# Kernel optimization log

Measured on AMD Instinct MI355X. Metric: run time of the kernel, lower is better.

The kernel has to match this reference:

```python
import jax, jax.numpy as jnp
import numpy as np

TEMPERATURE = 0.5


def _neg_indices(b):
    # Static (numpy) reconstruction of _get_correlated_mask for using_teacher=False:
    # mask excludes the diagonal and the +b/-b (mod 2b) positive-pair entries.
    n = 2 * b
    eye = np.eye(n, dtype=np.uint8)
    mask = (1 - (eye + np.roll(eye, -b, axis=1))).astype(bool)
    cols = np.broadcast_to(np.arange(n), (n, n))
    # torch's sim[mask].view(2b, -1) flattens row-major, so per-row sorted column order.
    return jnp.asarray(cols[mask].reshape(n, n - 2))  # [2b, 2b-2] int32


def setup_inputs() -> dict:
    key = jax.random.key(0)
    k1, k2 = jax.random.split(key)
    zis = jax.random.normal(k1, (4096, 256), dtype=jnp.float32)
    zjs = jax.random.normal(k2, (4096, 256), dtype=jnp.float32)
    return {"zis": zis, "zjs": zjs}


def reference(zis, zjs):
    b = zis.shape[0]
    reps = jnp.concatenate([zjs, zis], axis=0)              # [2b, d]
    sim = reps @ reps.T                                      # [2b, 2b] dot-product similarity
    # positives: sim[i, i+b] for i<b, then sim[i+b, i] -> sim[i, (i+b) mod 2b]
    l_pos = jnp.diagonal(sim, offset=b)
    r_pos = jnp.diagonal(sim, offset=-b)
    positives = jnp.concatenate([l_pos, r_pos])[:, None]     # [2b, 1]
    neg_idx = _neg_indices(b)
    negatives = jnp.take_along_axis(sim, neg_idx, axis=1)    # [2b, 2b-2]
    logits = jnp.concatenate([positives, negatives], axis=1) / TEMPERATURE
    # CrossEntropyLoss(reduction='sum') with labels all zero
    loss = jnp.sum(jax.nn.logsumexp(logits, axis=1) - logits[:, 0])
    accuracy = jnp.mean((jnp.argmax(logits, axis=1) == 0).astype(jnp.float32))
    return (loss / (2 * b), accuracy)
```

## Files before the change

kernel.cpp:

```cpp
#include <hip/hip_runtime.h>
#include <hip/hip_bf16.h>

#define N_TOT  8192
#define B_HALF 4096
#define D_DIM  256
#define NSPLIT 32
#define MFIX   192.0f

typedef short bf16x8 __attribute__((ext_vector_type(8)));
typedef float f32x4  __attribute__((ext_vector_type(4)));

#define NEG_INF (-__builtin_inff())
#define RSCALE  1.6986436f
#define LN2F    0.69314718056f

__device__ __forceinline__ float exp2_fast(float x) {
  float r;
  asm("v_exp_f32 %0, %1" : "=v"(r) : "v"(x));
  return r;
}

__device__ __forceinline__ unsigned short f2b(float f) {
  __hip_bfloat16 h = __float2bfloat16(f);
  return *reinterpret_cast<unsigned short*>(&h);
}

__global__ __launch_bounds__(256) void convert_k(const float* __restrict__ zis,
                                                 const float* __restrict__ zjs,
                                                 unsigned short* __restrict__ reps,
                                                 float* __restrict__ out) {
  size_t idx = ((size_t)blockIdx.x * 256 + threadIdx.x) * 4;
  const float* src = (idx < (size_t)B_HALF * D_DIM) ? (zjs + idx)
                                                    : (zis + (idx - (size_t)B_HALF * D_DIM));
  float4 v = *reinterpret_cast<const float4*>(src);
  ushort4 o;
  o.x = f2b(v.x * RSCALE); o.y = f2b(v.y * RSCALE);
  o.z = f2b(v.z * RSCALE); o.w = f2b(v.w * RSCALE);
  *reinterpret_cast<ushort4*>(reps + idx) = o;
  if (blockIdx.x == 0 && threadIdx.x < 2) out[threadIdx.x] = 0.0f;
}

#define G2L(srcp, ldsp)                                                          \
  __builtin_amdgcn_global_load_lds(                                              \
      (const __attribute__((address_space(1))) void*)(srcp),                     \
      (__attribute__((address_space(3))) void*)(ldsp), 16, 0, 0)

__global__ __launch_bounds__(512, 2) void ntxent_main(const unsigned short* __restrict__ reps,
                                                      float* __restrict__ part_m,
                                                      float* __restrict__ part_s,
                                                      float* __restrict__ pos_out) {
  __shared__ short As[2][16384];
  __shared__ short Bs[2][16384];

  const int tid  = threadIdx.x;
  const int lane = tid & 63;
  const int l15  = lane & 15;
  const int l4   = lane >> 4;
  const int wave = tid >> 6;
  const int wr   = wave >> 2;
  const int wc   = wave & 3;

  const unsigned wg = (blockIdx.x & 7) * 128 + (blockIdx.x >> 3);
  const int bx = wg >> 5, by = wg & 31;
  const int R0 = bx * 256, C0 = by * 256;
  const bool dblk = (bx == by);
  const bool pblk = (by == ((bx + 16) & 31));

#define ISSUE_A(h, slot, kt)                                                        \
  do {                                                                              \
    _Pragma("unroll") for (int j_ = 0; j_ < 2; ++j_) {                              \
      const int u_ = tid >> 3;                                                      \
      const unsigned short* s_ = reps + (size_t)(R0 + j_ * 128 + (h) * 64 + u_) * D_DIM \
                                 + (kt) * 64 + (((tid & 7) ^ (u_ & 7)) * 8);        \
      G2L(s_, &As[slot][(((h) * 2 + j_) * 512 + tid) * 8]);                         \
    }                                                                               \
  } while (0)

#define ISSUE_B(g, slot, kt)                                                        \
  do {                                                                              \
    _Pragma("unroll") for (int j_ = 0; j_ < 2; ++j_) {                              \
      const int u_ = tid >> 3;                                                      \
      const int col_ = (u_ & 31) + (g) * 32 + (((j_ * 2) + (u_ >> 5)) & 3) * 64;    \
      const unsigned short* s_ = reps + (size_t)(C0 + col_) * D_DIM                 \
                                 + (kt) * 64 + (((tid & 7) ^ (u_ & 7)) * 8);        \
      G2L(s_, &Bs[slot][(((g) * 2 + j_) * 512 + tid) * 8]);                         \
    }                                                                               \
  } while (0)

#define READ_A(h, slot)                                                             \
  do {                                                                              \
    _Pragma("unroll") for (int mf = 0; mf < 4; ++mf)                                \
      _Pragma("unroll") for (int kk = 0; kk < 2; ++kk)                              \
        af[mf][kk] = *reinterpret_cast<const bf16x8*>(                              \
            &As[slot][((h) * 128 + wr * 64 + mf * 16 + l15) * 64 +                  \
                      (((kk * 4 + l4) ^ (l15 & 7)) * 8)]);                          \
  } while (0)

#define READ_B(g, dst, slot)                                                        \
  do {                                                                              \
    _Pragma("unroll") for (int nf = 0; nf < 2; ++nf)                                \
      _Pragma("unroll") for (int kk = 0; kk < 2; ++kk)                              \
        dst[nf][kk] = *reinterpret_cast<const bf16x8*>(                             \
            &Bs[slot][((g) * 128 + wc * 32 + nf * 16 + l15) * 64 +                  \
                      (((kk * 4 + l4) ^ (l15 & 7)) * 8)]);                          \
  } while (0)

#define MFMA_Q(h, g, bfx)                                                           \
  do {                                                                              \
    _Pragma("unroll") for (int mf = 0; mf < 4; ++mf)                                \
      _Pragma("unroll") for (int nf = 0; nf < 2; ++nf)                              \
        _Pragma("unroll") for (int kk = 0; kk < 2; ++kk)                            \
          acc[h][g][mf][nf] = __builtin_amdgcn_mfma_f32_16x16x32_bf16(              \
              af[mf][kk], bfx[nf][kk], acc[h][g][mf][nf], 0, 0, 0);                 \
  } while (0)

#define PHASE_MID()                                          \
  do {                                                       \
    __builtin_amdgcn_s_barrier();                            \
    asm volatile("s_waitcnt lgkmcnt(0)" ::: "memory");       \
    __builtin_amdgcn_sched_barrier(0);                       \
    __builtin_amdgcn_s_setprio(1);                           \
  } while (0)

#define PHASE_END_G(n)                                       \
  do {                                                       \
    __builtin_amdgcn_s_setprio(0);                           \
    asm volatile("s_waitcnt vmcnt(" #n ")" ::: "memory");    \
    __builtin_amdgcn_s_barrier();                            \
  } while (0)

#define PHASE_END_NOG()                                      \
  do {                                                       \
    __builtin_amdgcn_s_setprio(0);                           \
    __builtin_amdgcn_s_barrier();                            \
  } while (0)

  f32x4 acc[2][2][4][2];
  const f32x4 vz = {0.f, 0.f, 0.f, 0.f};
#pragma unroll
  for (int h = 0; h < 2; ++h)
#pragma unroll
    for (int g = 0; g < 2; ++g)
#pragma unroll
      for (int mf = 0; mf < 4; ++mf)
#pragma unroll
        for (int nf = 0; nf < 2; ++nf) acc[h][g][mf][nf] = vz;

  bf16x8 af[4][2], bf0[2][2], bf1[2][2];

  ISSUE_A(0, 0, 0); ISSUE_B(0, 0, 0); ISSUE_B(1, 0, 0); ISSUE_A(1, 0, 0);
  asm volatile("s_waitcnt vmcnt(4)" ::: "memory");
  __builtin_amdgcn_s_barrier();

#pragma unroll
  for (int t = 0; t < 3; ++t) {
    const int sl = t & 1, sn = sl ^ 1, kn = t + 1;
    READ_A(0, sl); READ_B(0, bf0, sl); ISSUE_A(0, sn, kn);
    PHASE_MID(); MFMA_Q(0, 0, bf0); PHASE_END_G(4);
    READ_B(1, bf1, sl); ISSUE_B(0, sn, kn);
    PHASE_MID(); MFMA_Q(0, 1, bf1); PHASE_END_G(4);
    READ_A(1, sl); ISSUE_B(1, sn, kn);
    PHASE_MID(); MFMA_Q(1, 1, bf1); PHASE_END_NOG();
    ISSUE_A(1, sn, kn);
    PHASE_MID(); MFMA_Q(1, 0, bf0); PHASE_END_G(4);
  }
  READ_A(0, 1); READ_B(0, bf0, 1);
  PHASE_MID(); MFMA_Q(0, 0, bf0); PHASE_END_G(2);
  READ_B(1, bf1, 1);
  PHASE_MID(); MFMA_Q(0, 1, bf1); PHASE_END_G(0);
  READ_A(1, 1);
  PHASE_MID(); MFMA_Q(1, 1, bf1); PHASE_END_NOG();
  PHASE_MID(); MFMA_Q(1, 0, bf0);
  __builtin_amdgcn_s_setprio(0);

  __syncthreads();
  float2* red = reinterpret_cast<float2*>(&Bs[0][0]);
  float posv[2][4];
#pragma unroll
  for (int h = 0; h < 2; ++h)
#pragma unroll
    for (int mf = 0; mf < 4; ++mf) posv[h][mf] = NEG_INF;

#pragma unroll
  for (int h = 0; h < 2; ++h) {
#pragma unroll
    for (int mf = 0; mf < 4; ++mf) {
#pragma unroll
      for (int r = 0; r < 4; ++r) {
        float m_ = NEG_INF, s_ = 0.f;
#pragma unroll
        for (int g = 0; g < 2; ++g) {
#pragma unroll
          for (int nf = 0; nf < 2; ++nf) {
            float v = acc[h][g][mf][nf][r];
            const bool hit16 = (8 * wr + 4 * h + mf) == (4 * wc + 2 * g + nf);
            if (hit16 && l15 == l4 * 4 + r) {
              if (dblk) v = NEG_INF;
              if (pblk) posv[h][mf] = v;
            }
            m_ = fmaxf(m_, v);
            s_ += exp2_fast(v - MFIX);
          }
        }
#pragma unroll
        for (int off = 1; off < 16; off <<= 1) {
          s_ += __shfl_xor(s_, off, 16);
          m_ = fmaxf(m_, __shfl_xor(m_, off, 16));
        }
        if (l15 == 0)
          red[(wr * 128 + h * 64 + mf * 16 + l4 * 4 + r) * 4 + wc] = make_float2(m_, s_);
      }
    }
  }
  __syncthreads();
  if (tid < 256) {
    float2 p0 = red[tid * 4 + 0], p1 = red[tid * 4 + 1];
    float2 p2 = red[tid * 4 + 2], p3 = red[tid * 4 + 3];
    const int i = R0 + tid;
    part_m[i * NSPLIT + by] = fmaxf(fmaxf(p0.x, p1.x), fmaxf(p2.x, p3.x));
    part_s[i * NSPLIT + by] = p0.y + p1.y + p2.y + p3.y;
  }
  if (pblk) {
#pragma unroll
    for (int h = 0; h < 2; ++h) {
#pragma unroll
      for (int mf = 0; mf < 4; ++mf) {
        const bool valid = (unsigned)(8 * wr + 4 * h + mf - 4 * wc) < 4u;
#pragma unroll
        for (int r = 0; r < 4; ++r) {
          float p = __shfl(posv[h][mf], (lane & 48) + l4 * 4 + r, 64);
          if (valid && l15 == 0)
            pos_out[R0 + wr * 128 + h * 64 + mf * 16 + l4 * 4 + r] = p;
        }
      }
    }
  }
}

__global__ __launch_bounds__(256) void finalize_k(const float* __restrict__ pm,
                                                  const float* __restrict__ ps,
                                                  const float* __restrict__ pv,
                                                  float* __restrict__ out) {
  const int row = blockIdx.x * 256 + threadIdx.x;
  float m = NEG_INF, ss = 0.f;
#pragma unroll
  for (int s = 0; s < NSPLIT; ++s) {
    m  = fmaxf(m, pm[row * NSPLIT + s]);
    ss += ps[row * NSPLIT + s];
  }
  const float posu = pv[row];
  float loss = (MFIX + __log2f(ss) - posu) * LN2F;
  float hit  = (posu >= m) ? 1.0f : 0.0f;

#pragma unroll
  for (int off = 32; off; off >>= 1) {
    loss += __shfl_down(loss, off);
    hit  += __shfl_down(hit,  off);
  }
  __shared__ float redL[4], redH[4];
  const int wv = threadIdx.x >> 6;
  if ((threadIdx.x & 63) == 0) { redL[wv] = loss; redH[wv] = hit; }
  __syncthreads();
  if (threadIdx.x == 0) {
    float L = redL[0] + redL[1] + redL[2] + redL[3];
    float H = redH[0] + redH[1] + redH[2] + redH[3];
    atomicAdd(&out[0], L * (1.0f / 8192.0f));
    atomicAdd(&out[1], H * (1.0f / 8192.0f));
  }
}

extern "C" void kernel_launch(void* const* d_in, const int* in_sizes, int n_in,
                              void* d_out, int out_size, void* d_ws, size_t ws_size,
                              hipStream_t stream) {
  const float* zis = (const float*)d_in[0];
  const float* zjs = (const float*)d_in[1];
  float* out = (float*)d_out;

  char* ws = (char*)d_ws;
  unsigned short* reps = (unsigned short*)ws;
  float* part_m = (float*)(ws + 4u * 1024u * 1024u);
  float* part_s = (float*)(ws + 5u * 1024u * 1024u);
  float* pos_a  = (float*)(ws + 6u * 1024u * 1024u);
  (void)in_sizes; (void)n_in; (void)out_size; (void)ws_size;

  convert_k<<<2048, 256, 0, stream>>>(zis, zjs, reps, out);
  ntxent_main<<<1024, 512, 0, stream>>>(reps, part_m, part_s, pos_a);
  finalize_k<<<32, 256, 0, stream>>>(part_m, part_s, pos_a, out);
}
```

Measured before the change: 129.0 us.

## Make GEMM workgroups persistent over four column tiles and fuse finalize via last-block reduction

New measurement: 208.0 us. 1.61x slower.

```diff
diff --git a/kernel.cpp b/kernel.cpp
--- a/kernel.cpp
+++ b/kernel.cpp
@@ -4,7 +4,7 @@
 #define N_TOT  8192
 #define B_HALF 4096
 #define D_DIM  256
-#define NSPLIT 32
+#define PARTW  8
 #define MFIX   192.0f
 
 typedef short bf16x8 __attribute__((ext_vector_type(8)));
@@ -28,7 +28,8 @@
 __global__ __launch_bounds__(256) void convert_k(const float* __restrict__ zis,
                                                  const float* __restrict__ zjs,
                                                  unsigned short* __restrict__ reps,
-                                                 float* __restrict__ out) {
+                                                 float* __restrict__ out,
+                                                 int* __restrict__ counter) {
   size_t idx = ((size_t)blockIdx.x * 256 + threadIdx.x) * 4;
   const float* src = (idx < (size_t)B_HALF * D_DIM) ? (zjs + idx)
                                                     : (zis + (idx - (size_t)B_HALF * D_DIM));
@@ -38,6 +39,7 @@
   o.z = f2b(v.z * RSCALE); o.w = f2b(v.w * RSCALE);
   *reinterpret_cast<ushort4*>(reps + idx) = o;
   if (blockIdx.x == 0 && threadIdx.x < 2) out[threadIdx.x] = 0.0f;
+  if (blockIdx.x == 0 && threadIdx.x == 2) *counter = 0;
 }
 
 #define G2L(srcp, ldsp)                                                          \
@@ -48,9 +50,11 @@
 __global__ __launch_bounds__(512, 2) void ntxent_main(const unsigned short* __restrict__ reps,
                                                       float* __restrict__ part_m,
                                                       float* __restrict__ part_s,
-                                                      float* __restrict__ pos_out) {
-  __shared__ short As[2][16384];
-  __shared__ short Bs[2][16384];
+                                                      float* __restrict__ pos_out,
+                                                      int* __restrict__ counter,
+                                                      float* __restrict__ out) {
+  __shared__ short As[32768];
+  __shared__ short Bs[32768];
 
   const int tid  = threadIdx.x;
   const int lane = tid & 63;
@@ -60,49 +64,53 @@
   const int wr   = wave >> 2;
   const int wc   = wave & 3;
 
-  const unsigned wg = (blockIdx.x & 7) * 128 + (blockIdx.x >> 3);
-  const int bx = wg >> 5, by = wg & 31;
-  const int R0 = bx * 256, C0 = by * 256;
-  const bool dblk = (bx == by);
-  const bool pblk = (by == ((bx + 16) & 31));
-
-#define ISSUE_A(h, slot, kt)                                                        \
+  const int xcd  = (int)blockIdx.x & 7;
+  const int idx  = (int)blockIdx.x >> 3;
+  const int rp   = (xcd & 3) * 8 + (idx >> 2);
+  const int cg   = (xcd >> 2) * 4 + (idx & 3);
+  const int R0   = rp * 256;
+  const int G0   = cg * 1024;
+  const bool dblk = (cg == (rp >> 2));
+  const bool pblk = (cg == (((rp >> 2) + 4) & 7));
+  const int  sct  = rp & 3;
+
+#define ISSUE_A(hh, sbase, ko)                                                      \
   do {                                                                              \
     _Pragma("unroll") for (int j_ = 0; j_ < 2; ++j_) {                              \
       const int u_ = tid >> 3;                                                      \
-      const unsigned short* s_ = reps + (size_t)(R0 + j_ * 128 + (h) * 64 + u_) * D_DIM \
-                                 + (kt) * 64 + (((tid & 7) ^ (u_ & 7)) * 8);        \
-      G2L(s_, &As[slot][(((h) * 2 + j_) * 512 + tid) * 8]);                         \
+      const unsigned short* s_ = reps + (size_t)(R0 + j_ * 128 + (hh) * 64 + u_) * D_DIM \
+                                 + (ko) + (((tid & 7) ^ (u_ & 7)) * 8);             \
+      G2L(s_, (sbase) + (((hh) * 2 + j_) * 512 + tid) * 8);                         \
     }                                                                               \
   } while (0)
 
-#define ISSUE_B(g, slot, kt)                                                        \
+#define ISSUE_B(gg, sbase, cb, ko)                                                  \
   do {                                                                              \
     _Pragma("unroll") for (int j_ = 0; j_ < 2; ++j_) {                              \
       const int u_ = tid >> 3;                                                      \
-      const int col_ = (u_ & 31) + (g) * 32 + (((j_ * 2) + (u_ >> 5)) & 3) * 64;    \
-      const unsigned short* s_ = reps + (size_t)(C0 + col_) * D_DIM                 \
-                                 + (kt) * 64 + (((tid & 7) ^ (u_ & 7)) * 8);        \
-      G2L(s_, &Bs[slot][(((g) * 2 + j_) * 512 + tid) * 8]);                         \
+      const int col_ = (cb) + (u_ & 31) + (gg) * 32 + (((j_ * 2) + (u_ >> 5)) & 3) * 64; \
+      const unsigned short* s_ = reps + (size_t)col_ * D_DIM                        \
+                                 + (ko) + (((tid & 7) ^ (u_ & 7)) * 8);             \
+      G2L(s_, (sbase) + (((gg) * 2 + j_) * 512 + tid) * 8);                         \
     }                                                                               \
   } while (0)
 
-#define READ_A(h, slot)                                                             \
+#define READ_A(hh, sbase)                                                           \
   do {                                                                              \
     _Pragma("unroll") for (int mf = 0; mf < 4; ++mf)                                \
       _Pragma("unroll") for (int kk = 0; kk < 2; ++kk)                              \
         af[mf][kk] = *reinterpret_cast<const bf16x8*>(                              \
-            &As[slot][((h) * 128 + wr * 64 + mf * 16 + l15) * 64 +                  \
-                      (((kk * 4 + l4) ^ (l15 & 7)) * 8)]);                          \
-  } while (0)
-
-#define READ_B(g, dst, slot)                                                        \
+            (sbase) + ((hh) * 128 + wr * 64 + mf * 16 + l15) * 64 +                 \
+            (((kk * 4 + l4) ^ (l15 & 7)) * 8));                                     \
+  } while (0)
+
+#define READ_B(gg, dst, sbase)                                                      \
   do {                                                                              \
     _Pragma("unroll") for (int nf = 0; nf < 2; ++nf)                                \
       _Pragma("unroll") for (int kk = 0; kk < 2; ++kk)                              \
         dst[nf][kk] = *reinterpret_cast<const bf16x8*>(                             \
-            &Bs[slot][((g) * 128 + wc * 32 + nf * 16 + l15) * 64 +                  \
-                      (((kk * 4 + l4) ^ (l15 & 7)) * 8)]);                          \
+            (sbase) + ((gg) * 128 + wc * 32 + nf * 16 + l15) * 64 +                 \
+            (((kk * 4 + l4) ^ (l15 & 7)) * 8));                                     \
   } while (0)
 
 #define MFMA_Q(h, g, bfx)                                                           \
@@ -112,6 +120,26 @@
         _Pragma("unroll") for (int kk = 0; kk < 2; ++kk)                            \
           acc[h][g][mf][nf] = __builtin_amdgcn_mfma_f32_16x16x32_bf16(              \
               af[mf][kk], bfx[nf][kk], acc[h][g][mf][nf], 0, 0, 0);                 \
+  } while (0)
+
+#define EPI(h, g)                                                                   \
+  do {                                                                              \
+    _Pragma("unroll") for (int mf = 0; mf < 4; ++mf)                                \
+      _Pragma("unroll") for (int nf = 0; nf < 2; ++nf)                              \
+        _Pragma("unroll") for (int r = 0; r < 4; ++r) {                             \
+          float v = acc[h][g][mf][nf][r];                                           \
+          if (spec) {                                                               \
+            const bool own = ((8 * wr + 4 * (h) + mf) == (4 * wc + 2 * (g) + nf))   \
+                             && (l15 == l4 * 4 + r);                                \
+            if (own) {                                                              \
+              if (doD) v = NEG_INF;                                                 \
+              else pos_out[R0 + wr * 128 + (h) * 64 + mf * 16 + l15] = v;           \
+            }                                                                       \
+          }                                                                         \
+          m_st[h][mf][r] = fmaxf(m_st[h][mf][r], v);                                \
+          s_st[h][mf][r] += exp2_fast(v - MFIX);                                    \
+          acc[h][g][mf][nf][r] = 0.f;                                               \
+        }                                                                           \
   } while (0)
 
 #define PHASE_MID()                                          \
@@ -122,150 +150,155 @@
     __builtin_amdgcn_s_setprio(1);                           \
   } while (0)
 
-#define PHASE_END_G(n)                                       \
-  do {                                                       \
-    __builtin_amdgcn_s_setprio(0);                           \
-    asm volatile("s_waitcnt vmcnt(" #n ")" ::: "memory");    \
-    __builtin_amdgcn_s_barrier();                            \
-  } while (0)
-
-#define PHASE_END_NOG()                                      \
-  do {                                                       \
-    __builtin_amdgcn_s_setprio(0);                           \
-    __builtin_amdgcn_s_barrier();                            \
-  } while (0)
-
   f32x4 acc[2][2][4][2];
   const f32x4 vz = {0.f, 0.f, 0.f, 0.f};
+  float m_st[2][4][4], s_st[2][4][4];
 #pragma unroll
   for (int h = 0; h < 2; ++h)
 #pragma unroll
-    for (int g = 0; g < 2; ++g)
-#pragma unroll
-      for (int mf = 0; mf < 4; ++mf)
+    for (int mf = 0; mf < 4; ++mf) {
+#pragma unroll
+      for (int r = 0; r < 4; ++r) { m_st[h][mf][r] = NEG_INF; s_st[h][mf][r] = 0.f; }
+#pragma unroll
+      for (int g = 0; g < 2; ++g)
 #pragma unroll
         for (int nf = 0; nf < 2; ++nf) acc[h][g][mf][nf] = vz;
+    }
 
   bf16x8 af[4][2], bf0[2][2], bf1[2][2];
 
-  ISSUE_A(0, 0, 0); ISSUE_B(0, 0, 0); ISSUE_B(1, 0, 0); ISSUE_A(1, 0, 0);
+  ISSUE_A(0, As, 0); ISSUE_B(0, Bs, G0, 0); ISSUE_B(1, Bs, G0, 0); ISSUE_A(1, As, 0);
   asm volatile("s_waitcnt vmcnt(4)" ::: "memory");
   __builtin_amdgcn_s_barrier();
 
-#pragma unroll
-  for (int t = 0; t < 3; ++t) {
-    const int sl = t & 1, sn = sl ^ 1, kn = t + 1;
-    READ_A(0, sl); READ_B(0, bf0, sl); ISSUE_A(0, sn, kn);
-    PHASE_MID(); MFMA_Q(0, 0, bf0); PHASE_END_G(4);
-    READ_B(1, bf1, sl); ISSUE_B(0, sn, kn);
-    PHASE_MID(); MFMA_Q(0, 1, bf1); PHASE_END_G(4);
-    READ_A(1, sl); ISSUE_B(1, sn, kn);
-    PHASE_MID(); MFMA_Q(1, 1, bf1); PHASE_END_NOG();
-    ISSUE_A(1, sn, kn);
-    PHASE_MID(); MFMA_Q(1, 0, bf0); PHASE_END_G(4);
+  for (int it = 0; it < 15; ++it) {
+    const int ct = it >> 2;
+    const bool kt3 = (it & 3) == 3;
+    short* Ac = As + ((it & 1) << 14);
+    short* Bc = Bs + ((it & 1) << 14);
+    short* An = As + (((it & 1) ^ 1) << 14);
+    short* Bn = Bs + (((it & 1) ^ 1) << 14);
+    const int nko = ((it + 1) & 3) << 6;
+    const int ncb = G0 + ((it + 1) >> 2) * 256;
+    const bool doD = dblk && (ct == sct);
+    const bool doP = pblk && (ct == sct);
+    const bool spec = doD || doP;
+
+    READ_A(0, Ac); READ_B(0, bf0, Bc); ISSUE_A(0, An, nko);
+    PHASE_MID(); MFMA_Q(0, 0, bf0);
+    __builtin_amdgcn_s_setprio(0);
+    if (kt3) EPI(0, 0);
+    asm volatile("s_waitcnt vmcnt(4)" ::: "memory");
+    __builtin_amdgcn_s_barrier();
+    READ_B(1, bf1, Bc); ISSUE_B(0, Bn, ncb, nko);
+    PHASE_MID(); MFMA_Q(0, 1, bf1);
+    __builtin_amdgcn_s_setprio(0);
+    if (kt3) EPI(0, 1);
+    asm volatile("s_waitcnt vmcnt(4)" ::: "memory");
+    __builtin_amdgcn_s_barrier();
+    READ_A(1, Ac); ISSUE_B(1, Bn, ncb, nko);
+    PHASE_MID(); MFMA_Q(1, 1, bf1);
+    __builtin_amdgcn_s_setprio(0);
+    if (kt3) EPI(1, 1);
+    __builtin_amdgcn_s_barrier();
+    READ_B(0, bf0, Bc); ISSUE_A(1, An, nko);
+    PHASE_MID(); MFMA_Q(1, 0, bf0);
+    __builtin_amdgcn_s_setprio(0);
+    if (kt3) EPI(1, 0);
+    asm volatile("s_waitcnt vmcnt(4)" ::: "memory");
+    __builtin_amdgcn_s_barrier();
   }
-  READ_A(0, 1); READ_B(0, bf0, 1);
-  PHASE_MID(); MFMA_Q(0, 0, bf0); PHASE_END_G(2);
-  READ_B(1, bf1, 1);
-  PHASE_MID(); MFMA_Q(0, 1, bf1); PHASE_END_G(0);
-  READ_A(1, 1);
-  PHASE_MID(); MFMA_Q(1, 1, bf1); PHASE_END_NOG();
-  PHASE_MID(); MFMA_Q(1, 0, bf0);
-  __builtin_amdgcn_s_setprio(0);
-
+
+  {
+    const bool doD = dblk && (3 == sct);
+    const bool doP = pblk && (3 == sct);
+    const bool spec = doD || doP;
+    short* Ac = As + (1 << 14);
+    short* Bc = Bs + (1 << 14);
+    READ_A(0, Ac); READ_B(0, bf0, Bc);
+    PHASE_MID(); MFMA_Q(0, 0, bf0);
+    __builtin_amdgcn_s_setprio(0);
+    EPI(0, 0);
+    asm volatile("s_waitcnt vmcnt(2)" ::: "memory");
+    __builtin_amdgcn_s_barrier();
+    READ_B(1, bf1, Bc);
+    PHASE_MID(); MFMA_Q(0, 1, bf1);
+    __builtin_amdgcn_s_setprio(0);
+    EPI(0, 1);
+    asm volatile("s_waitcnt vmcnt(0)" ::: "memory");
+    __builtin_amdgcn_s_barrier();
+    READ_A(1, Ac);
+    PHASE_MID(); MFMA_Q(1, 1, bf1);
+    __builtin_amdgcn_s_setprio(0);
+    EPI(1, 1);
+    __builtin_amdgcn_s_barrier();
+    READ_B(0, bf0, Bc);
+    PHASE_MID(); MFMA_Q(1, 0, bf0);
+    __builtin_amdgcn_s_setprio(0);
+    EPI(1, 0);
+  }
   __syncthreads();
-  float2* red = reinterpret_cast<float2*>(&Bs[0][0]);
-  float posv[2][4];
+
+  float2* red = reinterpret_cast<float2*>(As);
 #pragma unroll
   for (int h = 0; h < 2; ++h)
 #pragma unroll
-    for (int mf = 0; mf < 4; ++mf) posv[h][mf] = NEG_INF;
-
-#pragma unroll
-  for (int h = 0; h < 2; ++h) {
-#pragma unroll
-    for (int mf = 0; mf < 4; ++mf) {
+    for (int mf = 0; mf < 4; ++mf)
 #pragma unroll
       for (int r = 0; r < 4; ++r) {
-        float m_ = NEG_INF, s_ = 0.f;
-#pragma unroll
-        for (int g = 0; g < 2; ++g) {
-#pragma unroll
-          for (int nf = 0; nf < 2; ++nf) {
-            float v = acc[h][g][mf][nf][r];
-            const bool hit16 = (8 * wr + 4 * h + mf) == (4 * wc + 2 * g + nf);
-            if (hit16 && l15 == l4 * 4 + r) {
-              if (dblk) v = NEG_INF;
-              if (pblk) posv[h][mf] = v;
-            }
-            m_ = fmaxf(m_, v);
-            s_ += exp2_fast(v - MFIX);
-          }
-        }
+        float s = s_st[h][mf][r], m = m_st[h][mf][r];
 #pragma unroll
         for (int off = 1; off < 16; off <<= 1) {
-          s_ += __shfl_xor(s_, off, 16);
-          m_ = fmaxf(m_, __shfl_xor(m_, off, 16));
+          s += __shfl_xor(s, off, 16);
+          m = fmaxf(m, __shfl_xor(m, off, 16));
         }
         if (l15 == 0)
-          red[(wr * 128 + h * 64 + mf * 16 + l4 * 4 + r) * 4 + wc] = make_float2(m_, s_);
+          red[(wr * 128 + h * 64 + mf * 16 + l4 * 4 + r) * 4 + wc] = make_float2(m, s);
       }
-    }
-  }
   __syncthreads();
   if (tid < 256) {
     float2 p0 = red[tid * 4 + 0], p1 = red[tid * 4 + 1];
     float2 p2 = red[tid * 4 + 2], p3 = red[tid * 4 + 3];
     const int i = R0 + tid;
-    part_m[i * NSPLIT + by] = fmaxf(fmaxf(p0.x, p1.x), fmaxf(p2.x, p3.x));
-    part_s[i * NSPLIT + by] = p0.y + p1.y + p2.y + p3.y;
+    part_m[i * PARTW + cg] = fmaxf(fmaxf(p0.x, p1.x), fmaxf(p2.x, p3.x));
+    part_s[i * PARTW + cg] = p0.y + p1.y + p2.y + p3.y;
   }
-  if (pblk) {
-#pragma unroll
-    for (int h = 0; h < 2; ++h) {
-#pragma unroll
-      for (int mf = 0; mf < 4; ++mf) {
-        const bool valid = (unsigned)(8 * wr + 4 * h + mf - 4 * wc) < 4u;
-#pragma unroll
-        for (int r = 0; r < 4; ++r) {
-          float p = __shfl(posv[h][mf], (lane & 48) + l4 * 4 + r, 64);
-          if (valid && l15 == 0)
-            pos_out[R0 + wr * 128 + h * 64 + mf * 16 + l4 * 4 + r] = p;
-        }
+
+  __threadfence();
+  __syncthreads();
+  __shared__ int isLast;
+  if (tid == 0) isLast = (atomicAdd(counter, 1) == 255) ? 1 : 0;
+  __syncthreads();
+  if (isLast) {
+    __threadfence();
+    float L = 0.f, H = 0.f;
+    for (int row = tid; row < N_TOT; row += 512) {
+      float m = NEG_INF, ss = 0.f;
+#pragma unroll
+      for (int c = 0; c < PARTW; ++c) {
+        m  = fmaxf(m, part_m[row * PARTW + c]);
+        ss += part_s[row * PARTW + c];
       }
+      const float pos = pos_out[row];
+      L += (MFIX + __log2f(ss) - pos);
+      H += (pos >= m) ? 1.0f : 0.0f;
     }
-  }
-}
-
-__global__ __launch_bounds__(256) void finalize_k(const float* __restrict__ pm,
-                                                  const float* __restrict__ ps,
-                                                  const float* __restrict__ pv,
-                                                  float* __restrict__ out) {
-  const int row = blockIdx.x * 256 + threadIdx.x;
-  float m = NEG_INF, ss = 0.f;
-#pragma unroll
-  for (int s = 0; s < NSPLIT; ++s) {
-    m  = fmaxf(m, pm[row * NSPLIT + s]);
-    ss += ps[row * NSPLIT + s];
-  }
-  const float posu = pv[row];
-  float loss = (MFIX + __log2f(ss) - posu) * LN2F;
-  float hit  = (posu >= m) ? 1.0f : 0.0f;
-
-#pragma unroll
-  for (int off = 32; off; off >>= 1) {
-    loss += __shfl_down(loss, off);
-    hit  += __shfl_down(hit,  off);
-  }
-  __shared__ float redL[4], redH[4];
-  const int wv = threadIdx.x >> 6;
-  if ((threadIdx.x & 63) == 0) { redL[wv] = loss; redH[wv] = hit; }
-  __syncthreads();
-  if (threadIdx.x == 0) {
-    float L = redL[0] + redL[1] + redL[2] + redL[3];
-    float H = redH[0] + redH[1] + redH[2] + redH[3];
-    atomicAdd(&out[0], L * (1.0f / 8192.0f));
-    atomicAdd(&out[1], H * (1.0f / 8192.0f));
+    L *= LN2F;
+#pragma unroll
+    for (int off = 32; off; off >>= 1) {
+      L += __shfl_down(L, off);
+      H += __shfl_down(H, off);
+    }
+    float* redf = reinterpret_cast<float*>(Bs);
+    if ((tid & 63) == 0) { redf[wave * 2] = L; redf[wave * 2 + 1] = H; }
+    __syncthreads();
+    if (tid == 0) {
+      float Lt = 0.f, Ht = 0.f;
+#pragma unroll
+      for (int w = 0; w < 8; ++w) { Lt += redf[w * 2]; Ht += redf[w * 2 + 1]; }
+      out[0] = Lt * (1.0f / 8192.0f);
+      out[1] = Ht * (1.0f / 8192.0f);
+    }
   }
 }
 
@@ -279,11 +312,11 @@
   char* ws = (char*)d_ws;
   unsigned short* reps = (unsigned short*)ws;
   float* part_m = (float*)(ws + 4u * 1024u * 1024u);
-  float* part_s = (float*)(ws + 5u * 1024u * 1024u);
-  float* pos_a  = (float*)(ws + 6u * 1024u * 1024u);
+  float* part_s = (float*)(ws + 4u * 1024u * 1024u + 256u * 1024u);
+  float* pos_a  = (float*)(ws + 4u * 1024u * 1024u + 512u * 1024u);
+  int*   cnt    = (int*)  (ws + 4u * 1024u * 1024u + 576u * 1024u);
   (void)in_sizes; (void)n_in; (void)out_size; (void)ws_size;
 
-  convert_k<<<2048, 256, 0, stream>>>(zis, zjs, reps, out);
-  ntxent_main<<<1024, 512, 0, stream>>>(reps, part_m, part_s, pos_a);
-  finalize_k<<<32, 256, 0, stream>>>(part_m, part_s, pos_a, out);
-}
+  convert_k<<<2048, 256, 0, stream>>>(zis, zjs, reps, out, cnt);
+  ntxent_main<<<256, 512, 0, stream>>>(reps, part_m, part_s, pos_a, cnt, out);
+}
```
